# Performance work log

Hardware: AMD Instinct MI355X
Metric: run time of the kernel (lower is better)

The kernel has to match this reference:

```python
import jax, jax.numpy as jnp
import numpy as np

B, C, H, W = 8, 256, 64, 64
IC = C // 2  # inter_channel


def setup_inputs() -> dict:
    key = jax.random.key(0)
    k0, k1, k2, k3, k4 = jax.random.split(key, 5)
    s = 0.05
    return {
        "x": jax.random.normal(k0, (B, C, H, W), dtype=jnp.float32),
        "w_theta": jax.random.normal(k1, (IC, C), dtype=jnp.float32) * s,
        "w_phi": jax.random.normal(k2, (IC, C), dtype=jnp.float32) * s,
        "w_g": jax.random.normal(k3, (IC, C), dtype=jnp.float32) * s,
        "w_mask": jax.random.normal(k4, (C, IC), dtype=jnp.float32) * s,
    }


def reference(x, w_theta, w_phi, w_g, w_mask):
    b, c, h, w = x.shape
    ic = c // 2
    # 1x1 convs (bias=False) == channel-mixing einsums -> (b, ic, h, w)
    theta = jnp.einsum("oc,bchw->bohw", w_theta, x)
    phi = jnp.einsum("oc,bchw->bohw", w_phi, x)
    g = jnp.einsum("oc,bchw->bohw", w_g, x)
    # Faithful to original: .view(b, c, -1) on a (b, ic, h, w) tensor
    # => sequence length N = h*w/2, feature dim = c (full channels).
    n = ic * h * w // c  # = h*w/2
    x_theta = theta.reshape(b, c, n).transpose(0, 2, 1)  # (b, n, c)
    x_phi = phi.reshape(b, c, n)                          # (b, c, n)
    x_g = g.reshape(b, c, n).transpose(0, 2, 1)           # (b, n, c)
    attn = jnp.matmul(x_theta, x_phi)                     # (b, n, n)
    # Original uses nn.Softmax(dim=1): normalize over ROWS, not last axis.
    attn = jax.nn.softmax(attn, axis=1)
    out = jnp.matmul(attn, x_g)                           # (b, n, c)
    out = out.transpose(0, 2, 1).reshape(b, ic, h, w)     # (b, ic, h, w)
    mask = jnp.einsum("oc,bchw->bohw", w_mask, out)       # (b, c, h, w)
    return mask + x
```

## Files before the change

### kernel.cpp

```cpp
#include <hip/hip_runtime.h>

typedef __attribute__((ext_vector_type(8))) __bf16 bf16x8;
typedef __attribute__((ext_vector_type(4))) float f32x4;

#define LOG2E 1.4426950408889634f

#define XT_OFF   0ul
#define OTA_OFF  0ul
#define TT_OFF   16777216ul
#define PT_OFF   25165824ul
#define G_OFF    33554432ul
#define W3_OFF   41943040ul
#define WM_OFF   42139648ul
#define ID_OFF   42205184ul
#define PART_OFF 42270720ul
#define WS_NEED  44367872ul

__device__ __forceinline__ void gload16(const __bf16* g, __bf16* l){
  __builtin_amdgcn_global_load_lds((const __attribute__((address_space(1))) void*)g,
                                   (__attribute__((address_space(3))) void*)l, 16, 0, 0);
}

__global__ __launch_bounds__(256) void k_weights(const float* wt, const float* wp,
                                                 const float* wg, const float* wm,
                                                 __bf16* W3, __bf16* Wm){
  int idx = blockIdx.x*256 + threadIdx.x;
  if (idx < 98304){
    float v = (idx < 32768) ? wt[idx] : (idx < 65536) ? wp[idx - 32768] : wg[idx - 65536];
    W3[idx] = (__bf16)v;
  } else if (idx < 131072){
    Wm[idx - 98304] = (__bf16)wm[idx - 98304];
  }
}

__global__ __launch_bounds__(256) void k_xt(const float* x, __bf16* Xt){
  __shared__ float tile[64][65];
  int b = blockIdx.z, c0 = blockIdx.y*64, p0 = blockIdx.x*64;
  int t = threadIdx.x, col = t & 63, r0 = t >> 6;
  const float* xb = x + ((size_t)b*256 + c0)*4096 + p0;
  #pragma unroll
  for (int rr = 0; rr < 16; ++rr){
    int row = rr*4 + r0;
    tile[row][col] = xb[(size_t)row*4096 + col];
  }
  __syncthreads();
  __bf16* xo = Xt + ((size_t)b*4096 + p0)*256 + c0;
  #pragma unroll
  for (int rr = 0; rr < 16; ++rr){
    int prow = rr*4 + r0;
    xo[(size_t)prow*256 + col] = (__bf16)tile[col][prow];
  }
}

__global__ __launch_bounds__(256) void k_conv3(const __bf16* Xt, const __bf16* W3,
                                               __bf16* Tt, __bf16* Pt, __bf16* G){
  __shared__ __bf16 As[128*72];
  __shared__ __bf16 Bs[64*72];
  int b = blockIdx.z, p0 = blockIdx.x*128, o0 = blockIdx.y*64;
  int tid = threadIdx.x, lane = tid & 63, wave = tid >> 6;
  int wm = wave >> 1, wn = wave & 1;
  f32x4 acc[4][2] = {};
  const __bf16* Ab = Xt + ((size_t)b*4096 + p0)*256;
  const __bf16* Bb = W3 + (size_t)o0*256;
  for (int kc = 0; kc < 4; ++kc){
    int k0 = kc*64;
    #pragma unroll
    for (int it = 0; it < 4; ++it){
      int s = tid + it*256, row = s >> 3, sk = s & 7;
      *(uint4*)&As[row*72 + sk*8] = *(const uint4*)(Ab + (size_t)row*256 + k0 + sk*8);
    }
    #pragma unroll
    for (int it = 0; it < 2; ++it){
      int s = tid + it*256, row = s >> 3, sk = s & 7;
      *(uint4*)&Bs[row*72 + sk*8] = *(const uint4*)(Bb + (size_t)row*256 + k0 + sk*8);
    }
    __syncthreads();
    #pragma unroll
    for (int ks = 0; ks < 2; ++ks){
      int koff = ks*32 + (lane>>4)*8;
      bf16x8 af[4], bfr[2];
      #pragma unroll
      for (int fm = 0; fm < 4; ++fm)
        af[fm] = *(const bf16x8*)&As[(wm*64 + fm*16 + (lane&15))*72 + koff];
      #pragma unroll
      for (int fn = 0; fn < 2; ++fn)
        bfr[fn] = *(const bf16x8*)&Bs[(wn*32 + fn*16 + (lane&15))*72 + koff];
      #pragma unroll
      for (int fm = 0; fm < 4; ++fm)
        #pragma unroll
        for (int fn = 0; fn < 2; ++fn)
          acc[fm][fn] = __builtin_amdgcn_mfma_f32_16x16x32_bf16(af[fm], bfr[fn], acc[fm][fn], 0, 0, 0);
    }
    __syncthreads();
  }
  #pragma unroll
  for (int fm = 0; fm < 4; ++fm)
    #pragma unroll
    for (int fn = 0; fn < 2; ++fn)
      #pragma unroll
      for (int r = 0; r < 4; ++r){
        int p = p0 + wm*64 + fm*16 + (lane>>4)*4 + r;
        int o = o0 + wn*32 + fn*16 + (lane&15);
        __bf16 v = (__bf16)acc[fm][fn][r];
        int i = p & 2047, ph = p >> 11;
        if (o < 128)      Tt[((size_t)b*2048 + i)*256 + 2*o + ph] = v;
        else if (o < 256) Pt[((size_t)b*2048 + i)*256 + 2*(o-128) + ph] = v;
        else              G [((size_t)b*256 + 2*(o-256) + ph)*2048 + i] = v;
      }
}

__global__ __launch_bounds__(512, 2) void k_sexp(const __bf16* Tt, const __bf16* Pt,
                                                 __bf16* S, float* PART, int js0){
  __shared__ __bf16 As[64*256];
  __shared__ __bf16 Bs[8][3][2048];
  int bid = blockIdx.x;
  int b = bid & 7, m = bid >> 3, m0 = m*64;
  int tid = threadIdx.x, lane = tid & 63, w = tid >> 6;
  int lr = lane & 15, kq = lane >> 4;
  const __bf16* Ab = Tt + ((size_t)b*2048 + m0)*256;
  const __bf16* Pb = Pt + ((size_t)b*2048 + js0)*256;
  __bf16* Sb = S + ((size_t)b*2048 + m0)*1024;
  {
    int aRow = lane >> 5, aSlot = lane & 31;
    #pragma unroll
    for (int u = 0; u < 4; ++u){
      int row = w*8 + u*2 + aRow;
      gload16(Ab + (size_t)row*256 + ((aSlot ^ (row & 7))*8), &As[w*2048 + u*512]);
    }
  }
  int bRow = lane >> 3, bSlot = lane & 7;
  #pragma unroll
  for (int s0 = 0; s0 < 2; ++s0){
    int j0 = (w + (s0 >> 2)*8)*32, kc = s0 & 3;
    #pragma unroll
    for (int u = 0; u < 4; ++u){
      int row = j0 + u*8 + bRow;
      gload16(Pb + (size_t)row*256 + kc*64 + ((bSlot ^ (row & 7))*8), &Bs[w][s0][u*512]);
    }
  }
  __syncthreads();
  bf16x8 aReg[4][8];
  #pragma unroll
  for (int fm = 0; fm < 4; ++fm){
    int ar = fm*16 + lr;
    #pragma unroll
    for (int sl = 0; sl < 8; ++sl){
      int slotA = (sl >> 1)*8 + (sl & 1)*4 + kq;
      aReg[fm][sl] = *(const bf16x8*)&As[ar*256 + ((slotA ^ (ar & 7))*8)];
    }
  }
  for (int q = 0; q < 4; ++q){
    int j0 = (w + q*8)*32;
    f32x4 acc[4][2] = {};
    #pragma unroll
    for (int kc = 0; kc < 4; ++kc){
      int s = q*4 + kc;
      if (s == 15) asm volatile("s_waitcnt vmcnt(0)" ::: "memory");
      else         asm volatile("s_waitcnt vmcnt(4)" ::: "memory");
      if (s + 2 < 16){
        int s2 = s + 2, q2 = s2 >> 2, kc2 = s2 & 3, rb = s2 % 3;
        int j02 = (w + q2*8)*32;
        #pragma unroll
        for (int u = 0; u < 4; ++u){
          int row = j02 + u*8 + bRow;
          gload16(Pb + (size_t)row*256 + kc2*64 + ((bSlot ^ (row & 7))*8), &Bs[w][rb][u*512]);
        }
      }
      const __bf16* Bc = &Bs[w][s % 3][0];
      #pragma unroll
      for (int ks = 0; ks < 2; ++ks){
        int slotB = ks*4 + kq;
        bf16x8 bf[2];
        #pragma unroll
        for (int fn = 0; fn < 2; ++fn){
          int br = fn*16 + lr;
          bf[fn] = *(const bf16x8*)&Bc[br*64 + ((slotB ^ (br & 7))*8)];
        }
        #pragma unroll
        for (int fm = 0; fm < 4; ++fm)
          #pragma unroll
          for (int fn = 0; fn < 2; ++fn)
            acc[fm][fn] = __builtin_amdgcn_mfma_f32_16x16x32_bf16(aReg[fm][kc*2+ks], bf[fn], acc[fm][fn], 0, 0, 0);
      }
    }
    #pragma unroll
    for (int fn = 0; fn < 2; ++fn){
      float v = 0.f;
      #pragma unroll
      for (int fm = 0; fm < 4; ++fm){
        #pragma unroll
        for (int r = 0; r < 4; ++r){
          float e = exp2f(acc[fm][fn][r] * LOG2E);
          v += e;
          Sb[(size_t)(fm*16 + kq*4 + r)*1024 + j0 + fn*16 + lr] = (__bf16)e;
        }
      }
      v += __shfl_xor(v, 16);
      v += __shfl_xor(v, 32);
      if (kq == 0)
        PART[((size_t)b*32 + m)*1024 + j0 + fn*16 + lr] = v;
    }
  }
}

__global__ __launch_bounds__(256) void k_invd(const float* PART, float* invD, int js0){
  int bid = blockIdx.x;
  int b = bid & 7, seg = bid >> 3;
  int jl = seg*256 + threadIdx.x;
  float s = 0.f;
  #pragma unroll
  for (int it = 0; it < 32; ++it) s += PART[((size_t)b*32 + it)*1024 + jl];
  invD[(size_t)b*2048 + js0 + jl] = 1.0f / s;
}

__global__ __launch_bounds__(256) void k_gscale(__bf16* G, const float* invD, int js0){
  int bid = blockIdx.x;
  int b = bid >> 8, c = bid & 255;
  int jl = threadIdx.x * 4;
  __bf16* gp = G + ((size_t)b*256 + c)*2048 + js0 + jl;
  const float* dp = invD + (size_t)b*2048 + js0 + jl;
  f32x4 d = *(const f32x4*)dp;
  __bf16 gv[4];
  *(uint2*)gv = *(const uint2*)gp;
  #pragma unroll
  for (int e = 0; e < 4; ++e) gv[e] = (__bf16)((float)gv[e] * d[e]);
  *(uint2*)gp = *(const uint2*)gv;
}

__global__ __launch_bounds__(256) void k_pv(const __bf16* S, const __bf16* G,
                                            float* OTacc, int js0, int first){
  __shared__ __bf16 sA[3][128*64];
  __shared__ __bf16 sB[3][64*64];
  int bid = blockIdx.x;
  int b = bid & 7, r2 = bid >> 3;
  int n = r2 & 3, m = r2 >> 2;
  int m0 = m*128, n0 = n*64;
  int tid = threadIdx.x, lane = tid & 63, w = tid >> 6;
  int lr = lane & 15, kq = lane >> 4;
  int wm = w >> 1, wn = w & 1;
  const __bf16* Ab = S + ((size_t)b*2048 + m0)*1024;
  const __bf16* Bb = G + ((size_t)b*256 + n0)*2048 + js0;
  int bRow = lane >> 3, bSlot = lane & 7;
  f32x4 acc[4][2] = {};
  #pragma unroll
  for (int t0 = 0; t0 < 2; ++t0){
    #pragma unroll
    for (int u = 0; u < 4; ++u){
      int row = u*32 + w*8 + bRow;
      gload16(Ab + (size_t)row*1024 + t0*64 + ((bSlot ^ (row & 7))*8),
              &sA[t0][u*2048 + w*512]);
    }
    #pragma unroll
    for (int u = 0; u < 2; ++u){
      int row = u*32 + w*8 + bRow;
      gload16(Bb + (size_t)row*2048 + t0*64 + ((bSlot ^ (row & 7))*8),
              &sB[t0][u*2048 + w*512]);
    }
  }
  for (int t = 0; t < 16; ++t){
    if (t == 15) asm volatile("s_waitcnt vmcnt(0)" ::: "memory");
    else         asm volatile("s_waitcnt vmcnt(6)" ::: "memory");
    __builtin_amdgcn_s_barrier();
    if (t + 2 < 16){
      int t2 = t + 2, bf2 = t2 % 3, k0 = t2*64;
      #pragma unroll
      for (int u = 0; u < 4; ++u){
        int row = u*32 + w*8 + bRow;
        gload16(Ab + (size_t)row*1024 + k0 + ((bSlot ^ (row & 7))*8),
                &sA[bf2][u*2048 + w*512]);
      }
      #pragma unroll
      for (int u = 0; u < 2; ++u){
        int row = u*32 + w*8 + bRow;
        gload16(Bb + (size_t)row*2048 + k0 + ((bSlot ^ (row & 7))*8),
                &sB[bf2][u*2048 + w*512]);
      }
    }
    const __bf16* Ac = &sA[t % 3][0];
    const __bf16* Bc = &sB[t % 3][0];
    #pragma unroll
    for (int ks = 0; ks < 2; ++ks){
      int slot = ks*4 + kq;
      bf16x8 af[4], bf[2];
      #pragma unroll
      for (int fm = 0; fm < 4; ++fm){
        int ar = wm*64 + fm*16 + lr;
        af[fm] = *(const bf16x8*)&Ac[ar*64 + ((slot ^ (ar & 7))*8)];
      }
      #pragma unroll
      for (int fn = 0; fn < 2; ++fn){
        int br = wn*32 + fn*16 + lr;
        bf[fn] = *(const bf16x8*)&Bc[br*64 + ((slot ^ (br & 7))*8)];
      }
      #pragma unroll
      for (int fm = 0; fm < 4; ++fm)
        #pragma unroll
        for (int fn = 0; fn < 2; ++fn)
          acc[fm][fn] = __builtin_amdgcn_mfma_f32_16x16x32_bf16(af[fm], bf[fn], acc[fm][fn], 0, 0, 0);
    }
  }
  float* Ob = OTacc + (size_t)b*4096*128;
  if (first){
    #pragma unroll
    for (int fm = 0; fm < 4; ++fm)
      #pragma unroll
      for (int fn = 0; fn < 2; ++fn)
        #pragma unroll
        for (int r = 0; r < 4; ++r){
          int i = m0 + wm*64 + fm*16 + kq*4 + r;
          int c = n0 + wn*32 + fn*16 + lr;
          Ob[(size_t)(((c & 1) << 11) + i)*128 + (c >> 1)] = acc[fm][fn][r];
        }
  } else {
    #pragma unroll
    for (int fm = 0; fm < 4; ++fm)
      #pragma unroll
      for (int fn = 0; fn < 2; ++fn)
        #pragma unroll
        for (int r = 0; r < 4; ++r){
          int i = m0 + wm*64 + fm*16 + kq*4 + r;
          int c = n0 + wn*32 + fn*16 + lr;
          size_t idx = (size_t)(((c & 1) << 11) + i)*128 + (c >> 1);
          Ob[idx] += acc[fm][fn][r];
        }
  }
}

__global__ __launch_bounds__(256) void k_mask(const float* OTacc, const __bf16* Wm,
                                              const float* x, float* out){
  __shared__ __bf16 As[128*72];
  __shared__ __bf16 Bs[64*72];
  int b = blockIdx.z, p0 = blockIdx.x*128, o0 = blockIdx.y*64;
  int tid = threadIdx.x, lane = tid & 63, wave = tid >> 6;
  int wm = wave >> 1, wn = wave & 1;
  f32x4 acc[4][2] = {};
  const float* Ab = OTacc + ((size_t)b*4096 + p0)*128;
  const __bf16* Bb = Wm + (size_t)o0*128;
  for (int kc = 0; kc < 2; ++kc){
    int k0 = kc*64;
    #pragma unroll
    for (int it = 0; it < 8; ++it){
      int idx = it*256 + tid;
      int row = idx >> 4, c4 = (idx & 15)*4;
      f32x4 vv = *(const f32x4*)(Ab + (size_t)row*128 + k0 + c4);
      __bf16 tmp[4];
      #pragma unroll
      for (int e = 0; e < 4; ++e) tmp[e] = (__bf16)vv[e];
      *(uint2*)&As[row*72 + c4] = *(const uint2*)tmp;
    }
    #pragma unroll
    for (int itc = 0; itc < 2; ++itc){
      int s = tid + itc*256, row = s >> 3, sk = s & 7;
      *(uint4*)&Bs[row*72 + sk*8] = *(const uint4*)(Bb + (size_t)row*128 + k0 + sk*8);
    }
    __syncthreads();
    #pragma unroll
    for (int ks = 0; ks < 2; ++ks){
      int koff = ks*32 + (lane>>4)*8;
      bf16x8 af[4], bfr[2];
      #pragma unroll
      for (int fm = 0; fm < 4; ++fm)
        af[fm] = *(const bf16x8*)&As[(wm*64 + fm*16 + (lane&15))*72 + koff];
      #pragma unroll
      for (int fn = 0; fn < 2; ++fn)
        bfr[fn] = *(const bf16x8*)&Bs[(wn*32 + fn*16 + (lane&15))*72 + koff];
      #pragma unroll
      for (int fm = 0; fm < 4; ++fm)
        #pragma unroll
        for (int fn = 0; fn < 2; ++fn)
          acc[fm][fn] = __builtin_amdgcn_mfma_f32_16x16x32_bf16(af[fm], bfr[fn], acc[fm][fn], 0, 0, 0);
    }
    __syncthreads();
  }
  #pragma unroll
  for (int fm = 0; fm < 4; ++fm)
    #pragma unroll
    for (int fn = 0; fn < 2; ++fn){
      int pb = p0 + wm*64 + fm*16 + (lane>>4)*4;
      int o = o0 + wn*32 + fn*16 + (lane&15);
      size_t idx = ((size_t)b*256 + o)*4096 + pb;
      f32x4 xv = *(const f32x4*)(x + idx);
      f32x4 ov = acc[fm][fn] + xv;
      *(f32x4*)(out + idx) = ov;
    }
}

extern "C" void kernel_launch(void* const* d_in, const int* in_sizes, int n_in,
                              void* d_out, int out_size, void* d_ws, size_t ws_size,
                              hipStream_t stream){
  if (ws_size < WS_NEED) return;
  const float* x  = (const float*)d_in[0];
  const float* wt = (const float*)d_in[1];
  const float* wp = (const float*)d_in[2];
  const float* wg = (const float*)d_in[3];
  const float* wm = (const float*)d_in[4];
  char* ws = (char*)d_ws;
  __bf16* Xt   = (__bf16*)(ws + XT_OFF);
  float* OTacc = (float*)(ws + OTA_OFF);
  __bf16* Tt   = (__bf16*)(ws + TT_OFF);
  __bf16* Pt   = (__bf16*)(ws + PT_OFF);
  __bf16* G    = (__bf16*)(ws + G_OFF);
  __bf16* W3   = (__bf16*)(ws + W3_OFF);
  __bf16* Wm   = (__bf16*)(ws + WM_OFF);
  float* invD  = (float*)(ws + ID_OFF);
  float* PART  = (float*)(ws + PART_OFF);
  __bf16* S    = (__bf16*)d_out;
  float* out   = (float*)d_out;

  k_weights<<<512, 256, 0, stream>>>(wt, wp, wg, wm, W3, Wm);
  k_xt<<<dim3(64, 4, 8), 256, 0, stream>>>(x, Xt);
  k_conv3<<<dim3(32, 6, 8), 256, 0, stream>>>(Xt, W3, Tt, Pt, G);
  for (int s = 0; s < 2; ++s){
    int js0 = s * 1024;
    k_sexp<<<256, 512, 0, stream>>>(Tt, Pt, S, PART, js0);
    k_invd<<<32, 256, 0, stream>>>(PART, invD, js0);
    k_gscale<<<2048, 256, 0, stream>>>(G, invD, js0);
    k_pv<<<512, 256, 0, stream>>>(S, G, OTacc, js0, s == 0 ? 1 : 0);
  }
  k_mask<<<dim3(32, 4, 8), 256, 0, stream>>>(OTacc, Wm, x, out);
}
```

Measured before the change: 149.3 us.

## Fuse x transpose/bf16 cast into projection GEMM with resident A tile

Removes the separate transpose kernel that wrote a bf16 copy of x to workspace. The new conv kernel reads fp32 x directly and transposes it through a small LDS tile into a swizzled, block-resident A tile, which is then held in registers. It then loops over all six output-channel tiles, double-buffering the weights with async global-to-LDS loads. This saves a kernel launch and a full write-then-read of Xt. In exchange it uses 256 larger blocks, heavy register use for the A fragments, and more LDS, which may lower occupancy and parallelism.

```diff
diff --git a/kernel.cpp b/kernel.cpp
--- a/kernel.cpp
+++ b/kernel.cpp
@@ -5,7 +5,6 @@
 
 #define LOG2E 1.4426950408889634f
 
-#define XT_OFF   0ul
 #define OTA_OFF  0ul
 #define TT_OFF   16777216ul
 #define PT_OFF   25165824ul
@@ -33,80 +32,93 @@
   }
 }
 
-__global__ __launch_bounds__(256) void k_xt(const float* x, __bf16* Xt){
-  __shared__ float tile[64][65];
-  int b = blockIdx.z, c0 = blockIdx.y*64, p0 = blockIdx.x*64;
-  int t = threadIdx.x, col = t & 63, r0 = t >> 6;
-  const float* xb = x + ((size_t)b*256 + c0)*4096 + p0;
-  #pragma unroll
-  for (int rr = 0; rr < 16; ++rr){
-    int row = rr*4 + r0;
-    tile[row][col] = xb[(size_t)row*4096 + col];
-  }
-  __syncthreads();
-  __bf16* xo = Xt + ((size_t)b*4096 + p0)*256 + c0;
-  #pragma unroll
-  for (int rr = 0; rr < 16; ++rr){
-    int prow = rr*4 + r0;
-    xo[(size_t)prow*256 + col] = (__bf16)tile[col][prow];
-  }
-}
-
-__global__ __launch_bounds__(256) void k_conv3(const __bf16* Xt, const __bf16* W3,
-                                               __bf16* Tt, __bf16* Pt, __bf16* G){
-  __shared__ __bf16 As[128*72];
-  __shared__ __bf16 Bs[64*72];
-  int b = blockIdx.z, p0 = blockIdx.x*128, o0 = blockIdx.y*64;
-  int tid = threadIdx.x, lane = tid & 63, wave = tid >> 6;
-  int wm = wave >> 1, wn = wave & 1;
-  f32x4 acc[4][2] = {};
-  const __bf16* Ab = Xt + ((size_t)b*4096 + p0)*256;
-  const __bf16* Bb = W3 + (size_t)o0*256;
-  for (int kc = 0; kc < 4; ++kc){
-    int k0 = kc*64;
-    #pragma unroll
-    for (int it = 0; it < 4; ++it){
-      int s = tid + it*256, row = s >> 3, sk = s & 7;
-      *(uint4*)&As[row*72 + sk*8] = *(const uint4*)(Ab + (size_t)row*256 + k0 + sk*8);
-    }
-    #pragma unroll
-    for (int it = 0; it < 2; ++it){
-      int s = tid + it*256, row = s >> 3, sk = s & 7;
-      *(uint4*)&Bs[row*72 + sk*8] = *(const uint4*)(Bb + (size_t)row*256 + k0 + sk*8);
+__global__ __launch_bounds__(512, 2) void k_conv3x(const float* x, const __bf16* W3,
+                                                   __bf16* Tt, __bf16* Pt, __bf16* G){
+  __shared__ __bf16 As[128*256];
+  __shared__ __bf16 Bs[2][64*256];
+  __shared__ float  tf[64*65];
+  int bid = blockIdx.x;
+  int b = bid & 7, m = bid >> 3, p0 = m*128;
+  int tid = threadIdx.x, lane = tid & 63, w = tid >> 6;
+  int lr = lane & 15, kq = lane >> 4;
+  int pw = w & 1, ow4 = w >> 1;
+  const float* xb = x + (size_t)b*256*4096 + p0;
+  int sRow2 = lane >> 5, sSlot = lane & 31;
+  #pragma unroll
+  for (int u = 0; u < 4; ++u){
+    int row = u*16 + w*2 + sRow2;
+    gload16(W3 + (size_t)row*256 + ((sSlot ^ (row & 7))*8), &Bs[0][(u*16 + w*2)*256]);
+  }
+  #pragma unroll
+  for (int st = 0; st < 8; ++st){
+    int ct = st >> 1, pt = st & 1;
+    int c0 = ct*64, ps = pt*64;
+    #pragma unroll
+    for (int u = 0; u < 2; ++u){
+      int idx = u*512 + tid;
+      int row = idx >> 4, col4 = (idx & 15)*4;
+      f32x4 v = *(const f32x4*)(xb + (size_t)(c0 + row)*4096 + ps + col4);
+      #pragma unroll
+      for (int e = 0; e < 4; ++e) tf[row*65 + col4 + e] = v[e];
     }
     __syncthreads();
-    #pragma unroll
-    for (int ks = 0; ks < 2; ++ks){
-      int koff = ks*32 + (lane>>4)*8;
-      bf16x8 af[4], bfr[2];
-      #pragma unroll
-      for (int fm = 0; fm < 4; ++fm)
-        af[fm] = *(const bf16x8*)&As[(wm*64 + fm*16 + (lane&15))*72 + koff];
-      #pragma unroll
-      for (int fn = 0; fn < 2; ++fn)
-        bfr[fn] = *(const bf16x8*)&Bs[(wn*32 + fn*16 + (lane&15))*72 + koff];
-      #pragma unroll
-      for (int fm = 0; fm < 4; ++fm)
-        #pragma unroll
-        for (int fn = 0; fn < 2; ++fn)
-          acc[fm][fn] = __builtin_amdgcn_mfma_f32_16x16x32_bf16(af[fm], bfr[fn], acc[fm][fn], 0, 0, 0);
+    {
+      int pl = tid & 63, slot8 = tid >> 6;
+      __bf16 pk[8];
+      #pragma unroll
+      for (int e = 0; e < 8; ++e) pk[e] = (__bf16)tf[(slot8*8 + e)*65 + pl];
+      int row = ps + pl, slotIdx = ct*8 + slot8;
+      *(uint4*)&As[row*256 + ((slotIdx ^ (row & 7))*8)] = *(const uint4*)pk;
     }
     __syncthreads();
   }
-  #pragma unroll
-  for (int fm = 0; fm < 4; ++fm)
-    #pragma unroll
-    for (int fn = 0; fn < 2; ++fn)
+  bf16x8 aReg[4][8];
+  #pragma unroll
+  for (int fm = 0; fm < 4; ++fm){
+    int ar = pw*64 + fm*16 + lr;
+    #pragma unroll
+    for (int sl = 0; sl < 8; ++sl){
+      int slotA = (sl >> 1)*8 + (sl & 1)*4 + kq;
+      aReg[fm][sl] = *(const bf16x8*)&As[ar*256 + ((slotA ^ (ar & 7))*8)];
+    }
+  }
+  for (int ot = 0; ot < 6; ++ot){
+    if (ot < 5){
+      int buf = (ot + 1) & 1;
+      #pragma unroll
+      for (int u = 0; u < 4; ++u){
+        int row = u*16 + w*2 + sRow2;
+        gload16(W3 + (size_t)((ot+1)*64 + row)*256 + ((sSlot ^ (row & 7))*8),
+                &Bs[buf][(u*16 + w*2)*256]);
+      }
+    }
+    const __bf16* Bc = &Bs[ot & 1][0];
+    f32x4 acc[4] = {};
+    #pragma unroll
+    for (int kc = 0; kc < 4; ++kc)
+      #pragma unroll
+      for (int ks = 0; ks < 2; ++ks){
+        int slotB = kc*8 + ks*4 + kq;
+        int br = ow4*16 + lr;
+        bf16x8 bf = *(const bf16x8*)&Bc[br*256 + ((slotB ^ (br & 7))*8)];
+        #pragma unroll
+        for (int fm = 0; fm < 4; ++fm)
+          acc[fm] = __builtin_amdgcn_mfma_f32_16x16x32_bf16(aReg[fm][kc*2+ks], bf, acc[fm], 0, 0, 0);
+      }
+    #pragma unroll
+    for (int fm = 0; fm < 4; ++fm)
       #pragma unroll
       for (int r = 0; r < 4; ++r){
-        int p = p0 + wm*64 + fm*16 + (lane>>4)*4 + r;
-        int o = o0 + wn*32 + fn*16 + (lane&15);
-        __bf16 v = (__bf16)acc[fm][fn][r];
+        int p = p0 + pw*64 + fm*16 + kq*4 + r;
+        int o = ot*64 + ow4*16 + lr;
+        __bf16 v = (__bf16)acc[fm][r];
         int i = p & 2047, ph = p >> 11;
         if (o < 128)      Tt[((size_t)b*2048 + i)*256 + 2*o + ph] = v;
         else if (o < 256) Pt[((size_t)b*2048 + i)*256 + 2*(o-128) + ph] = v;
         else              G [((size_t)b*256 + 2*(o-256) + ph)*2048 + i] = v;
       }
+    __syncthreads();
+  }
 }
 
 __global__ __launch_bounds__(512, 2) void k_sexp(const __bf16* Tt, const __bf16* Pt,
@@ -395,7 +407,6 @@
   const float* wg = (const float*)d_in[3];
   const float* wm = (const float*)d_in[4];
   char* ws = (char*)d_ws;
-  __bf16* Xt   = (__bf16*)(ws + XT_OFF);
   float* OTacc = (float*)(ws + OTA_OFF);
   __bf16* Tt   = (__bf16*)(ws + TT_OFF);
   __bf16* Pt   = (__bf16*)(ws + PT_OFF);
@@ -408,8 +419,7 @@
   float* out   = (float*)d_out;
 
   k_weights<<<512, 256, 0, stream>>>(wt, wp, wg, wm, W3, Wm);
-  k_xt<<<dim3(64, 4, 8), 256, 0, stream>>>(x, Xt);
-  k_conv3<<<dim3(32, 6, 8), 256, 0, stream>>>(Xt, W3, Tt, Pt, G);
+  k_conv3x<<<256, 512, 0, stream>>>(x, W3, Tt, Pt, G);
   for (int s = 0; s < 2; ++s){
     int js0 = s * 1024;
     k_sexp<<<256, 512, 0, stream>>>(Tt, Pt, S, PART, js0);
```

Measured after the change: 134.7 us. -9.8%, faster.
